# Optimization experiments

Hardware: AMD Instinct MI355X
Metric: run time of the kernel (lower is better)

Reference implementation:

```python
import jax, jax.numpy as jnp
import numpy as np

N_KEYS, PER_KEY = 8, 6
NUM_CONCEPTS = N_KEYS * PER_KEY  # 48
NUM_CLASS = 7
D_VIT, D = 768, 512
LOGIT_SCALE = 100.0


def adaptive_avg_pool_matrix(L_in: int, L_out: int) -> np.ndarray:
    """Linear operator replicating torch AdaptiveAvgPool1d: out[i] = mean(x[start_i:end_i])."""
    M = np.zeros((L_in, L_out), dtype=np.float32)
    for i in range(L_out):
        s = (i * L_in) // L_out
        e = -(((-(i + 1)) * L_in) // L_out)  # ceil((i+1)*L_in/L_out)
        M[s:e, i] = 1.0 / (e - s)
    return M


def setup_inputs() -> dict:
    key = jax.random.key(0)
    ks = jax.random.split(key, 12)
    feats = jax.random.normal(ks[0], (12, 32, 197, D_VIT), dtype=jnp.float32)
    # frozen text-side concept embeddings (CLIP text feats are ~unit norm, 512-d)
    ce = jax.random.normal(ks[1], (NUM_CONCEPTS, D), dtype=jnp.float32)
    concept_embeds = ce / jnp.linalg.norm(ce, axis=-1, keepdims=True)
    sc = 1.0 / np.sqrt(D_VIT)
    W_lin = jax.random.normal(ks[2], (D, D_VIT), dtype=jnp.float32) * sc
    b_lin = jnp.zeros((D,), dtype=jnp.float32)
    W_proj = jax.random.normal(ks[3], (D, D_VIT), dtype=jnp.float32) * sc
    scg = 1.0 / np.sqrt(3 * D)
    W_gate = jax.random.normal(ks[4], (D, 3 * D), dtype=jnp.float32) * scg
    b_gate = jnp.zeros((D,), dtype=jnp.float32)
    scu = 1.0 / np.sqrt(2 * D)
    W_upd = jax.random.normal(ks[5], (D, 2 * D), dtype=jnp.float32) * scu
    b_upd = jnp.zeros((D,), dtype=jnp.float32)
    W_cls = jax.random.normal(ks[6], (NUM_CLASS, NUM_CONCEPTS), dtype=jnp.float32) / np.sqrt(NUM_CONCEPTS)
    b_cls = jnp.zeros((NUM_CLASS,), dtype=jnp.float32)
    return {
        'feats': feats, 'concept_embeds': concept_embeds,
        'W_lin': W_lin, 'b_lin': b_lin, 'W_proj': W_proj,
        'W_gate': W_gate, 'b_gate': b_gate, 'W_upd': W_upd, 'b_upd': b_upd,
        'W_cls': W_cls, 'b_cls': b_cls,
    }


def _forward(feats, concept_embeds, W_lin, b_lin, W_proj, W_gate, b_gate, W_upd, b_upd, W_cls, b_cls):
    L, B, S, _ = feats.shape
    M = jnp.asarray(adaptive_avg_pool_matrix(S - 1, NUM_CONCEPTS))  # [196, 48]
    q0 = jnp.broadcast_to(concept_embeds[None], (B, NUM_CONCEPTS, D))

    def step(q, f):  # f: [B, 197, 768]
        cls_tok = f[:, :1, :]                                  # [B,1,768]
        pooled = jnp.einsum('bjd,ji->bid', f[:, 1:, :], M)     # [B,48,768]
        vt = jnp.concatenate([cls_tok, pooled], axis=1) @ W_lin.T + b_lin  # [B,49,512]
        attn = jax.nn.softmax(jnp.einsum('bqd,bvd->bqv', q, vt), axis=-1)
        fuse = jnp.einsum('bqv,bvd->bqd', attn, vt)            # [B,48,512]
        cls_ctx = jnp.broadcast_to(cls_tok @ W_proj.T, q.shape)
        gate = jax.nn.sigmoid(jnp.concatenate([fuse, q, cls_ctx], -1) @ W_gate.T + b_gate)
        upd = jnp.tanh(jnp.concatenate([fuse, q], -1) @ W_upd.T + b_upd)
        return gate * q + (1.0 - gate) * upd, fuse

    _, trace = jax.lax.scan(step, q0, feats)                   # trace: [12,B,48,512]

    last = trace[-1]
    vision_semantic = last / jnp.maximum(jnp.linalg.norm(last, axis=-1, keepdims=True), 1e-12)
    vs = vision_semantic.reshape(B, N_KEYS, PER_KEY, D)
    anchors = concept_embeds.reshape(N_KEYS, PER_KEY, D)
    image_logits = (LOGIT_SCALE * jnp.einsum('bkpd,kqd->bkpq', vs, anchors).mean(axis=2)).reshape(B, NUM_CONCEPTS)
    cls_logits = image_logits @ W_cls.T + b_cls
    diffs = trace[1:] - jax.lax.stop_gradient(trace[:-1])
    loss_consistency = jnp.sum(jnp.mean(diffs * diffs, axis=(1, 2, 3)))
    return cls_logits, image_logits, loss_consistency


def reference(feats, concept_embeds, W_lin, b_lin, W_proj, W_gate, b_gate, W_upd, b_upd, W_cls, b_cls):
    return _forward(feats, concept_embeds, W_lin, b_lin, W_proj, W_gate, b_gate, W_upd, b_upd, W_cls, b_cls)
```

## Files before the change

### kernel.cpp

```cpp
#include <hip/hip_runtime.h>
#include <hip/hip_bf16.h>

#define LL 12
#define BB 32
#define SS 197
#define DV 768
#define DD 512
#define CC 48
#define VV 49
#define LOSS_DEN 786432.0f

typedef unsigned short u16;
typedef unsigned int u32;
using bf16x8 = __attribute__((ext_vector_type(8))) __bf16;
using f32x4 = __attribute__((ext_vector_type(4))) float;
using u16x8 = __attribute__((ext_vector_type(8))) u16;

__device__ __forceinline__ u16 bf16h(float x) {
    u32 u = __builtin_bit_cast(u32, x);
    return (u16)((u + 0x7FFFu + ((u >> 16) & 1u)) >> 16);
}
__device__ __forceinline__ float bf2f(u16 h) {
    u32 u = ((u32)h) << 16;
    return __builtin_bit_cast(float, u);
}
__device__ __forceinline__ f32x4 mfma16(bf16x8 a, bf16x8 b, f32x4 c) {
    return __builtin_amdgcn_mfma_f32_16x16x32_bf16(a, b, c, 0, 0, 0);
}
__device__ __forceinline__ void gl_lds16(const void* g, void* s) {
    __builtin_amdgcn_global_load_lds((const __attribute__((address_space(1))) u32*)g,
                                     (__attribute__((address_space(3))) u32*)s, 16, 0, 0);
}

#define NLW (512 * 768)
#define NGW (512 * 1536)
#define NUW (512 * 1024)
#define POOL_BLKS (LL * BB * VV)
#define WSPLIT_BLKS ((NLW + NGW + NUW) / 256)
#define INITQ_BLKS ((BB * CC * DD) / 256)

__global__ __launch_bounds__(256) void mega_pre(const float* __restrict__ feats,
                                                const float* __restrict__ Wl,
                                                const float* __restrict__ Wg,
                                                const float* __restrict__ Wu,
                                                const float* __restrict__ ce,
                                                u16* __restrict__ Xh, u16* __restrict__ Xl,
                                                u16* Wlh, u16* Wll, u16* Wgh, u16* Wgl,
                                                u16* Wuh, u16* Wul,
                                                u16* __restrict__ qh, u16* __restrict__ ql,
                                                float* __restrict__ loss) {
    int bid = blockIdx.x;
    int t = threadIdx.x;
    if (bid < POOL_BLKS) {
        int row = bid;
        int v = row % VV;
        int lb = row / VV;
        const float* f = feats + (size_t)lb * SS * DV;
        for (int d = t; d < DV; d += 256) {
            float val;
            if (v == 0) {
                val = f[d];
            } else {
                int i = v - 1;
                int s = (i * 196) / 48;
                int e = ((i + 1) * 196 + 47) / 48;
                float acc = 0.0f;
                for (int j = s; j < e; ++j) acc += f[(size_t)(1 + j) * DV + d];
                val = acc / (float)(e - s);
            }
            u16 h = bf16h(val);
            Xh[(size_t)row * DV + d] = h;
            Xl[(size_t)row * DV + d] = bf16h(val - bf2f(h));
        }
    } else if (bid < POOL_BLKS + WSPLIT_BLKS) {
        int i = (bid - POOL_BLKS) * 256 + t;
        float v;
        u16 *ph, *pl;
        int j;
        if (i < NLW) { v = Wl[i]; ph = Wlh; pl = Wll; j = i; }
        else if (i < NLW + NGW) { j = i - NLW; v = Wg[j]; ph = Wgh; pl = Wgl; }
        else { j = i - NLW - NGW; v = Wu[j]; ph = Wuh; pl = Wul; }
        u16 hh = bf16h(v);
        ph[j] = hh;
        pl[j] = bf16h(v - bf2f(hh));
    } else {
        int i = (bid - POOL_BLKS - WSPLIT_BLKS) * 256 + t;
        float v = ce[i % (CC * DD)];
        u16 hh = bf16h(v);
        qh[i] = hh;
        ql[i] = bf16h(v - bf2f(hh));
        if (i == 0) loss[0] = 0.0f;
    }
}

__global__ __launch_bounds__(256) void gemm_f32(const float* __restrict__ A, int lda,
                                                const float* __restrict__ W, int wstride, int K,
                                                const float* __restrict__ bias,
                                                float* __restrict__ Cout) {
    __shared__ float As[32][65];
    __shared__ float Bs[32][65];
    int t = threadIdx.x;
    int m0 = blockIdx.x * 64;
    int n0 = blockIdx.y * 64;
    int r = t >> 2;
    int kc = (t & 3) * 8;
    int tx = t & 15, ty = t >> 4;
    float acc[4][4] = {};
    for (int k0 = 0; k0 < K; k0 += 32) {
        const float4* pa = (const float4*)(A + (size_t)(m0 + r) * lda + k0 + kc);
        float4 a0 = pa[0], a1 = pa[1];
        const float4* pw = (const float4*)(W + (size_t)(n0 + r) * wstride + k0 + kc);
        float4 w0 = pw[0], w1 = pw[1];
        As[kc + 0][r] = a0.x; As[kc + 1][r] = a0.y; As[kc + 2][r] = a0.z; As[kc + 3][r] = a0.w;
        As[kc + 4][r] = a1.x; As[kc + 5][r] = a1.y; As[kc + 6][r] = a1.z; As[kc + 7][r] = a1.w;
        Bs[kc + 0][r] = w0.x; Bs[kc + 1][r] = w0.y; Bs[kc + 2][r] = w0.z; Bs[kc + 3][r] = w0.w;
        Bs[kc + 4][r] = w1.x; Bs[kc + 5][r] = w1.y; Bs[kc + 6][r] = w1.z; Bs[kc + 7][r] = w1.w;
        __syncthreads();
#pragma unroll
        for (int kk = 0; kk < 32; ++kk) {
            float a[4], b[4];
#pragma unroll
            for (int i = 0; i < 4; ++i) { a[i] = As[kk][ty * 4 + i]; b[i] = Bs[kk][tx * 4 + i]; }
#pragma unroll
            for (int i = 0; i < 4; ++i)
#pragma unroll
                for (int j = 0; j < 4; ++j) acc[i][j] += a[i] * b[j];
        }
        __syncthreads();
    }
#pragma unroll
    for (int i = 0; i < 4; ++i) {
        int m = m0 + ty * 4 + i;
#pragma unroll
        for (int j = 0; j < 4; ++j) {
            int n = n0 + tx * 4 + j;
            Cout[(size_t)m * DD + n] = acc[i][j] + (bias ? bias[n] : 0.0f);
        }
    }
}

__global__ __launch_bounds__(256, 2) void vt_gemm(const u16* __restrict__ Xh, const u16* __restrict__ Xl,
                                                  const u16* __restrict__ Wh, const u16* __restrict__ Wl,
                                                  const float* __restrict__ bias,
                                                  u16* __restrict__ vthp, u16* __restrict__ vtlp) {
    __shared__ u16 sm[24576];
    int tid = threadIdx.x;
    int w = tid >> 6, l = tid & 63, lr = l & 15, ls = l >> 4;
    int i = blockIdx.x, m, n;
    if (i < 1152) { int a = i >> 6, r2 = i & 63; m = 8 * a + (r2 & 7); n = r2 >> 3; }
    else { int j = i - 1152; m = 144 + (j >> 3); n = j & 7; }
    int m0 = m * 128, n0 = n * 64;
    f32x4 acc[2][4];
#pragma unroll
    for (int ii = 0; ii < 2; ++ii)
#pragma unroll
        for (int j = 0; j < 4; ++j) acc[ii][j] = f32x4{0.f, 0.f, 0.f, 0.f};

    auto stage = [&](u16* dst, int k0) {
#pragma unroll
        for (int is = 0; is < 6; ++is) {
            int q = is * 256 + tid;
            const u16* src;
            int off;
            if (is < 2)      { int qr = q;        int row = qr >> 2, sl = qr & 3; src = Xh + (size_t)(m0 + row) * DV + k0 + ((sl ^ ((row >> 1) & 3)) << 3); off = qr * 8; }
            else if (is < 4) { int qr = q - 512;  int row = qr >> 2, sl = qr & 3; src = Xl + (size_t)(m0 + row) * DV + k0 + ((sl ^ ((row >> 1) & 3)) << 3); off = 4096 + qr * 8; }
            else if (is < 5) { int qr = q - 1024; int row = qr >> 2, sl = qr & 3; src = Wh + (size_t)(n0 + row) * DV + k0 + ((sl ^ ((row >> 1) & 3)) << 3); off = 8192 + qr * 8; }
            else             { int qr = q - 1280; int row = qr >> 2, sl = qr & 3; src = Wl + (size_t)(n0 + row) * DV + k0 + ((sl ^ ((row >> 1) & 3)) << 3); off = 10240 + qr * 8; }
            gl_lds16(src, dst + off);
        }
    };

    stage(sm, 0);
    __syncthreads();
    for (int t = 0; t < 24; ++t) {
        u16* cur = sm + ((t & 1) ? 12288 : 0);
        u16* nxt = sm + ((t & 1) ? 0 : 12288);
        if (t + 1 < 24) stage(nxt, (t + 1) * 32);
        bf16x8 ah[2], al2[2], bh[4], bl2[4];
#pragma unroll
        for (int rf = 0; rf < 2; ++rf) {
            int row = 32 * w + 16 * rf + lr;
            int ro = row * 32 + ((ls ^ ((row >> 1) & 3)) << 3);
            ah[rf] = *(const bf16x8*)(cur + ro);
            al2[rf] = *(const bf16x8*)(cur + 4096 + ro);
        }
#pragma unroll
        for (int cf = 0; cf < 4; ++cf) {
            int nn = 16 * cf + lr;
            int no = nn * 32 + ((ls ^ ((nn >> 1) & 3)) << 3);
            bh[cf] = *(const bf16x8*)(cur + 8192 + no);
            bl2[cf] = *(const bf16x8*)(cur + 10240 + no);
        }
#pragma unroll
        for (int rf = 0; rf < 2; ++rf)
#pragma unroll
            for (int cf = 0; cf < 4; ++cf) {
                acc[rf][cf] = mfma16(ah[rf], bh[cf], acc[rf][cf]);
                acc[rf][cf] = mfma16(ah[rf], bl2[cf], acc[rf][cf]);
                acc[rf][cf] = mfma16(al2[rf], bh[cf], acc[rf][cf]);
            }
        __syncthreads();
    }
#pragma unroll
    for (int rf = 0; rf < 2; ++rf)
#pragma unroll
        for (int cf = 0; cf < 4; ++cf)
#pragma unroll
            for (int r = 0; r < 4; ++r) {
                int row = m0 + 32 * w + 16 * rf + 4 * ls + r;
                int col = n0 + 16 * cf + lr;
                float v = acc[rf][cf][r] + bias[col];
                size_t o = (size_t)row * DD + col;
                u16 hh = bf16h(v);
                vthp[o] = hh;
                vtlp[o] = bf16h(v - bf2f(hh));
            }
}

__device__ __forceinline__ void gemm32x64(u16* sm, const u16* Ah, const u16* Al,
                                          const u16* Wgh, const u16* Wgl,
                                          const u16* Wuh, const u16* Wul,
                                          int m0, int n0, int colOff, int tid,
                                          f32x4 accg[2], f32x4 accu[2]) {
    int w = tid >> 6, lane = tid & 63, lr = lane & 15, ls = lane >> 4;
    auto stage = [&](u16* buf, int k0) {
        {
            int j = tid, row = j >> 3, sl = j & 7;
            int ko = k0 + ((sl ^ (row & 7)) << 3);
            gl_lds16(Ah + (size_t)(m0 + row) * DD + ko, buf + j * 8);
            gl_lds16(Al + (size_t)(m0 + row) * DD + ko, buf + 2048 + j * 8);
        }
#pragma unroll
        for (int i2 = 0; i2 < 8; ++i2) {
            int aidx = tid + 256 * i2;
            int arr = aidx >> 9, j = aidx & 511;
            int row = j >> 3, sl = j & 7;
            int ko = colOff + k0 + ((sl ^ (row & 7)) << 3);
            const u16* src;
            if (arr == 0) src = Wgh + (size_t)(n0 + row) * 1536 + ko;
            else if (arr == 1) src = Wgl + (size_t)(n0 + row) * 1536 + ko;
            else if (arr == 2) src = Wuh + (size_t)(n0 + row) * 1024 + ko;
            else src = Wul + (size_t)(n0 + row) * 1024 + ko;
            gl_lds16(src, buf + 4096 + arr * 4096 + j * 8);
        }
    };
    stage(sm, 0);
    __syncthreads();
    for (int t = 0; t < 8; ++t) {
        u16* cur = sm + (t & 1) * 20480;
        if (t + 1 < 8) stage(sm + ((t + 1) & 1) * 20480, (t + 1) * 64);
#pragma unroll
        for (int ks = 0; ks < 2; ++ks) {
            int slot = ks * 4 + ls;
            int n = 16 * w + lr;
            int bo = n * 64 + ((slot ^ (n & 7)) << 3);
            bf16x8 gh8 = *(const bf16x8*)(cur + 4096 + bo);
            bf16x8 gl8 = *(const bf16x8*)(cur + 8192 + bo);
            bf16x8 uh8 = *(const bf16x8*)(cur + 12288 + bo);
            bf16x8 ul8 = *(const bf16x8*)(cur + 16384 + bo);
#pragma unroll
            for (int rf = 0; rf < 2; ++rf) {
                int r = 16 * rf + lr;
                int ao = r * 64 + ((slot ^ (r & 7)) << 3);
                bf16x8 ah8 = *(const bf16x8*)(cur + ao);
                bf16x8 al8 = *(const bf16x8*)(cur + 2048 + ao);
                accg[rf] = mfma16(ah8, gh8, accg[rf]);
                accg[rf] = mfma16(ah8, gl8, accg[rf]);
                accg[rf] = mfma16(al8, gh8, accg[rf]);
                accu[rf] = mfma16(ah8, uh8, accu[rf]);
                accu[rf] = mfma16(ah8, ul8, accu[rf]);
                accu[rf] = mfma16(al8, uh8, accu[rf]);
            }
        }
        __syncthreads();
    }
}

__global__ __launch_bounds__(256, 2) void attn_qpart(
    const u16* __restrict__ qh, const u16* __restrict__ ql,
    const u16* __restrict__ vthL, const u16* __restrict__ vtlL,
    float* __restrict__ fcur, const float* __restrict__ fprev,
    u16* __restrict__ fh, u16* __restrict__ fl,
    float* __restrict__ loss, int do_loss,
    const u16* __restrict__ Wgh, const u16* __restrict__ Wgl,
    const u16* __restrict__ Wuh, const u16* __restrict__ Wul,
    float* __restrict__ qg, float* __restrict__ qu) {
    __shared__ u16 sm[40960];
    int tid = threadIdx.x;
    if (blockIdx.x < 192) {
        int wgid = blockIdx.x * 4 + (tid >> 6);
        int lane = tid & 63;
        int b = wgid / 24;
        int r0 = b * CC + (wgid % 24) * 2;
        size_t o0 = (size_t)r0 * DD + lane * 8;
        u16x8 h0 = *(const u16x8*)(qh + o0), g0 = *(const u16x8*)(ql + o0);
        u16x8 h1 = *(const u16x8*)(qh + o0 + DD), g1 = *(const u16x8*)(ql + o0 + DD);
        float q0v[8], q1v[8];
#pragma unroll
        for (int j = 0; j < 8; ++j) {
            q0v[j] = bf2f(h0[j]) + bf2f(g0[j]);
            q1v[j] = bf2f(h1[j]) + bf2f(g1[j]);
        }
        const u16* vh = vthL + (size_t)b * VV * DD + lane * 8;
        const u16* vl = vtlL + (size_t)b * VV * DD + lane * 8;
        float m0 = -3e38f, m1 = -3e38f, s0 = 0.f, s1 = 0.f;
        float a0[8] = {}, a1[8] = {};
        for (int v = 0; v < VV; ++v) {
            u16x8 rh = *(const u16x8*)(vh + v * DD);
            u16x8 rl = *(const u16x8*)(vl + v * DD);
            float rv[8];
#pragma unroll
            for (int j = 0; j < 8; ++j) rv[j] = bf2f(rh[j]) + bf2f(rl[j]);
            float p0 = 0.f, p1 = 0.f;
#pragma unroll
            for (int j = 0; j < 8; ++j) { p0 += q0v[j] * rv[j]; p1 += q1v[j] * rv[j]; }
#pragma unroll
            for (int off = 32; off > 0; off >>= 1) { p0 += __shfl_xor(p0, off); p1 += __shfl_xor(p1, off); }
            float nm0 = fmaxf(m0, p0);
            float sc0 = __expf(m0 - nm0), w0 = __expf(p0 - nm0);
            s0 = s0 * sc0 + w0;
            float nm1 = fmaxf(m1, p1);
            float sc1 = __expf(m1 - nm1), w1 = __expf(p1 - nm1);
            s1 = s1 * sc1 + w1;
#pragma unroll
            for (int j = 0; j < 8; ++j) {
                a0[j] = a0[j] * sc0 + w0 * rv[j];
                a1[j] = a1[j] * sc1 + w1 * rv[j];
            }
            m0 = nm0;
            m1 = nm1;
        }
        float inv0 = 1.0f / s0, inv1 = 1.0f / s1;
        float d2 = 0.f;
        float f0v[8], f1v[8];
        u16x8 oh0, ol0, oh1, ol1;
#pragma unroll
        for (int j = 0; j < 8; ++j) {
            float f = a0[j] * inv0;
            f0v[j] = f;
            u16 hh = bf16h(f);
            oh0[j] = hh;
            ol0[j] = bf16h(f - bf2f(hh));
            float f2 = a1[j] * inv1;
            f1v[j] = f2;
            u16 h2 = bf16h(f2);
            oh1[j] = h2;
            ol1[j] = bf16h(f2 - bf2f(h2));
        }
        *(float4*)(fcur + o0) = float4{f0v[0], f0v[1], f0v[2], f0v[3]};
        *(float4*)(fcur + o0 + 4) = float4{f0v[4], f0v[5], f0v[6], f0v[7]};
        *(float4*)(fcur + o0 + DD) = float4{f1v[0], f1v[1], f1v[2], f1v[3]};
        *(float4*)(fcur + o0 + DD + 4) = float4{f1v[4], f1v[5], f1v[6], f1v[7]};
        *(u16x8*)(fh + o0) = oh0;
        *(u16x8*)(fl + o0) = ol0;
        *(u16x8*)(fh + o0 + DD) = oh1;
        *(u16x8*)(fl + o0 + DD) = ol1;
        if (do_loss) {
#pragma unroll
            for (int j = 0; j < 8; ++j) {
                float d = f0v[j] - fprev[o0 + j];
                d2 += d * d;
                float e = f1v[j] - fprev[o0 + DD + j];
                d2 += e * e;
            }
#pragma unroll
            for (int off = 32; off > 0; off >>= 1) d2 += __shfl_xor(d2, off);
            if (lane == 0) atomicAdd(loss, d2);
        }
    } else {
        int tb = blockIdx.x - 192;
        int m0 = (tb >> 3) * 32, n0 = (tb & 7) * 64;
        f32x4 accg[2], accu[2];
#pragma unroll
        for (int i = 0; i < 2; ++i) { accg[i] = f32x4{0.f, 0.f, 0.f, 0.f}; accu[i] = f32x4{0.f, 0.f, 0.f, 0.f}; }
        gemm32x64(sm, qh, ql, Wgh, Wgl, Wuh, Wul, m0, n0, 512, tid, accg, accu);
        int w = tid >> 6, lane = tid & 63, lr = lane & 15, ls = lane >> 4;
#pragma unroll
        for (int rf = 0; rf < 2; ++rf)
#pragma unroll
            for (int r = 0; r < 4; ++r) {
                int row = m0 + 16 * rf + 4 * ls + r;
                int col = n0 + 16 * w + lr;
                size_t o = (size_t)row * DD + col;
                qg[o] = accg[rf][r];
                qu[o] = accu[rf][r];
            }
    }
}

__global__ __launch_bounds__(256, 2) void fusepart(
    const u16* __restrict__ fhp, const u16* __restrict__ flp,
    const u16* __restrict__ qhp, const u16* __restrict__ qlp,
    const u16* __restrict__ Wgh, const u16* __restrict__ Wgl,
    const u16* __restrict__ Wuh, const u16* __restrict__ Wul,
    const float* __restrict__ qg, const float* __restrict__ qu,
    const float* __restrict__ CgL, const float* __restrict__ bu,
    u16* __restrict__ qoh, u16* __restrict__ qol) {
    __shared__ u16 sm[40960];
    int tid = threadIdx.x;
    int m0 = (blockIdx.x >> 3) * 32, n0 = (blockIdx.x & 7) * 64;
    f32x4 accg[2], accu[2];
#pragma unroll
    for (int i = 0; i < 2; ++i) { accg[i] = f32x4{0.f, 0.f, 0.f, 0.f}; accu[i] = f32x4{0.f, 0.f, 0.f, 0.f}; }
    gemm32x64(sm, fhp, flp, Wgh, Wgl, Wuh, Wul, m0, n0, 0, tid, accg, accu);
    int w = tid >> 6, lane = tid & 63, lr = lane & 15, ls = lane >> 4;
#pragma unroll
    for (int rf = 0; rf < 2; ++rf)
#pragma unroll
        for (int r = 0; r < 4; ++r) {
            int row = m0 + 16 * rf + 4 * ls + r;
            int col = n0 + 16 * w + lr;
            int b = row / CC;
            size_t o = (size_t)row * DD + col;
            float gpre = accg[rf][r] + qg[o] + CgL[(size_t)b * DD + col];
            float upre = accu[rf][r] + qu[o] + bu[col];
            float g = 1.0f / (1.0f + __expf(-gpre));
            float u = tanhf(upre);
            float qv = bf2f(qhp[o]) + bf2f(qlp[o]);
            float qo = g * qv + (1.0f - g) * u;
            u16 hh = bf16h(qo);
            qoh[o] = hh;
            qol[o] = bf16h(qo - bf2f(hh));
        }
}

__global__ __launch_bounds__(256) void final_kernel(const float* __restrict__ fuse_last,
                                                    const float* __restrict__ ce,
                                                    const float* __restrict__ W_cls,
                                                    const float* __restrict__ b_cls,
                                                    const float* __restrict__ loss_acc,
                                                    float* __restrict__ out) {
    int b = blockIdx.x;
    int t = threadIdx.x;
    int w = t >> 6, lane = t & 63;
    __shared__ float invn[CC];
    __shared__ float img[CC];
    const float* fb = fuse_last + (size_t)b * CC * DD;
    for (int c = w; c < CC; c += 4) {
        const float* fr = fb + (size_t)c * DD + lane * 8;
        float4 a0 = *(const float4*)fr;
        float4 a1 = *(const float4*)(fr + 4);
        float ss = a0.x * a0.x + a0.y * a0.y + a0.z * a0.z + a0.w * a0.w +
                   a1.x * a1.x + a1.y * a1.y + a1.z * a1.z + a1.w * a1.w;
#pragma unroll
        for (int off = 32; off > 0; off >>= 1) ss += __shfl_xor(ss, off);
        if (lane == 0) invn[c] = 1.0f / fmaxf(sqrtf(ss), 1e-12f);
    }
    __syncthreads();
    for (int g = w; g < CC; g += 4) {
        int k = g / 6;
        const float* ar = ce + (size_t)g * DD + lane * 8;
        float4 c0 = *(const float4*)ar;
        float4 c1 = *(const float4*)(ar + 4);
        float av[8] = {c0.x, c0.y, c0.z, c0.w, c1.x, c1.y, c1.z, c1.w};
        float accp = 0.0f;
        for (int p = 0; p < 6; ++p) {
            int row = k * 6 + p;
            const float* fr = fb + (size_t)row * DD + lane * 8;
            float4 f0 = *(const float4*)fr;
            float4 f1 = *(const float4*)(fr + 4);
            float fv[8] = {f0.x, f0.y, f0.z, f0.w, f1.x, f1.y, f1.z, f1.w};
            float d = 0.0f;
#pragma unroll
            for (int j = 0; j < 8; ++j) d += fv[j] * av[j];
            accp += d * invn[row];
        }
#pragma unroll
        for (int off = 32; off > 0; off >>= 1) accp += __shfl_xor(accp, off);
        if (lane == 0) img[g] = accp * (100.0f / 6.0f);
    }
    __syncthreads();
    if (t < CC) out[BB * 7 + b * CC + t] = img[t];
    if (t < 7) {
        float sacc = b_cls[t];
        for (int c = 0; c < CC; ++c) sacc += img[c] * W_cls[t * CC + c];
        out[b * 7 + t] = sacc;
    }
    if (b == 0 && t == 0) out[BB * 7 + BB * CC] = loss_acc[0] * (1.0f / LOSS_DEN);
}

extern "C" void kernel_launch(void* const* d_in, const int* in_sizes, int n_in,
                              void* d_out, int out_size, void* d_ws, size_t ws_size,
                              hipStream_t stream) {
    const float* feats = (const float*)d_in[0];
    const float* ce = (const float*)d_in[1];
    const float* W_lin = (const float*)d_in[2];
    const float* b_lin = (const float*)d_in[3];
    const float* W_proj = (const float*)d_in[4];
    const float* W_gate = (const float*)d_in[5];
    const float* b_gate = (const float*)d_in[6];
    const float* W_upd = (const float*)d_in[7];
    const float* b_upd = (const float*)d_in[8];
    const float* W_cls = (const float*)d_in[9];
    const float* b_cls = (const float*)d_in[10];
    float* out = (float*)d_out;

    char* base = (char*)d_ws;
    size_t off = 0;
    auto alloc = [&](size_t bytes) -> char* {
        char* r = base + off;
        off += (bytes + 255) & ~(size_t)255;
        return r;
    };
    u16* Xh = (u16*)alloc((size_t)LL * BB * VV * DV * 2);
    u16* Xl = (u16*)alloc((size_t)LL * BB * VV * DV * 2);
    u16* vth = (u16*)alloc((size_t)LL * BB * VV * DD * 2);
    u16* vtl = (u16*)alloc((size_t)LL * BB * VV * DD * 2);
    float* ctx = (float*)alloc((size_t)LL * BB * DD * 4);
    float* Cg = (float*)alloc((size_t)LL * BB * DD * 4);
    float* fbuf0 = (float*)alloc((size_t)BB * CC * DD * 4);
    float* fbuf1 = (float*)alloc((size_t)BB * CC * DD * 4);
    float* qg = (float*)alloc((size_t)BB * CC * DD * 4);
    float* qu = (float*)alloc((size_t)BB * CC * DD * 4);
    float* loss = (float*)alloc(256);
    u16* Wlh = (u16*)alloc((size_t)NLW * 2);
    u16* Wll = (u16*)alloc((size_t)NLW * 2);
    u16* Wgh = (u16*)alloc((size_t)NGW * 2);
    u16* Wgl = (u16*)alloc((size_t)NGW * 2);
    u16* Wuh = (u16*)alloc((size_t)NUW * 2);
    u16* Wul = (u16*)alloc((size_t)NUW * 2);
    u16* fh = (u16*)alloc((size_t)BB * CC * DD * 2);
    u16* fl = (u16*)alloc((size_t)BB * CC * DD * 2);
    u16* qah = (u16*)alloc((size_t)BB * CC * DD * 2);
    u16* qal = (u16*)alloc((size_t)BB * CC * DD * 2);
    u16* qbh = (u16*)alloc((size_t)BB * CC * DD * 2);
    u16* qbl = (u16*)alloc((size_t)BB * CC * DD * 2);
    u16* qph[2] = {qah, qbh};
    u16* qpl[2] = {qal, qbl};

    mega_pre<<<POOL_BLKS + WSPLIT_BLKS + INITQ_BLKS, 256, 0, stream>>>(
        feats, W_lin, W_gate, W_upd, ce, Xh, Xl, Wlh, Wll, Wgh, Wgl, Wuh, Wul, qah, qal, loss);
    {
        dim3 g(LL * BB / 64, DD / 64);
        gemm_f32<<<g, 256, 0, stream>>>(feats, SS * DV, W_proj, DV, DV, nullptr, ctx);
        gemm_f32<<<g, 256, 0, stream>>>(ctx, DD, W_gate + 1024, 1536, DD, b_gate, Cg);
    }
    vt_gemm<<<1176, 256, 0, stream>>>(Xh, Xl, Wlh, Wll, b_lin, vth, vtl);

    int qc = 0;
    for (int l = 0; l < LL; ++l) {
        float* fcur = (l & 1) ? fbuf1 : fbuf0;
        const float* fprev = (l & 1) ? fbuf0 : fbuf1;
        int grid = (l < LL - 1) ? 576 : 192;
        attn_qpart<<<grid, 256, 0, stream>>>(qph[qc], qpl[qc],
                                             vth + (size_t)l * BB * VV * DD, vtl + (size_t)l * BB * VV * DD,
                                             fcur, fprev, fh, fl, loss, l > 0 ? 1 : 0,
                                             Wgh, Wgl, Wuh, Wul, qg, qu);
        if (l < LL - 1) {
            fusepart<<<384, 256, 0, stream>>>(fh, fl, qph[qc], qpl[qc],
                                              Wgh, Wgl, Wuh, Wul, qg, qu,
                                              Cg + (size_t)l * BB * DD, b_upd,
                                              qph[qc ^ 1], qpl[qc ^ 1]);
            qc ^= 1;
        }
    }

    final_kernel<<<BB, 256, 0, stream>>>((LL - 1) & 1 ? fbuf1 : fbuf0, ce, W_cls, b_cls, loss, out);
}
```

Before: 940.2 us.

## Fold ctx/Cg GEMMs into pre and vt kernels; one query row per wavefront

New measurement: 2.781 ms. 2.96x slower.

```diff
diff --git a/kernel.cpp b/kernel.cpp
--- a/kernel.cpp
+++ b/kernel.cpp
@@ -38,17 +38,65 @@
 #define POOL_BLKS (LL * BB * VV)
 #define WSPLIT_BLKS ((NLW + NGW + NUW) / 256)
 #define INITQ_BLKS ((BB * CC * DD) / 256)
+#define CTX_BLKS 48
+
+__device__ __forceinline__ void gemm_f32_tile(const float* __restrict__ A, int lda,
+                                              const float* __restrict__ W, int wstride, int K,
+                                              const float* __restrict__ bias,
+                                              float* __restrict__ Cout,
+                                              int m0, int n0, int t, float* AsB, float* BsB) {
+    float (*As)[65] = (float(*)[65])AsB;
+    float (*Bs)[65] = (float(*)[65])BsB;
+    int r = t >> 2;
+    int kc = (t & 3) * 8;
+    int tx = t & 15, ty = t >> 4;
+    float acc[4][4] = {};
+    for (int k0 = 0; k0 < K; k0 += 32) {
+        const float4* pa = (const float4*)(A + (size_t)(m0 + r) * lda + k0 + kc);
+        float4 a0 = pa[0], a1 = pa[1];
+        const float4* pw = (const float4*)(W + (size_t)(n0 + r) * wstride + k0 + kc);
+        float4 w0 = pw[0], w1 = pw[1];
+        As[kc + 0][r] = a0.x; As[kc + 1][r] = a0.y; As[kc + 2][r] = a0.z; As[kc + 3][r] = a0.w;
+        As[kc + 4][r] = a1.x; As[kc + 5][r] = a1.y; As[kc + 6][r] = a1.z; As[kc + 7][r] = a1.w;
+        Bs[kc + 0][r] = w0.x; Bs[kc + 1][r] = w0.y; Bs[kc + 2][r] = w0.z; Bs[kc + 3][r] = w0.w;
+        Bs[kc + 4][r] = w1.x; Bs[kc + 5][r] = w1.y; Bs[kc + 6][r] = w1.z; Bs[kc + 7][r] = w1.w;
+        __syncthreads();
+#pragma unroll
+        for (int kk = 0; kk < 32; ++kk) {
+            float a[4], b[4];
+#pragma unroll
+            for (int i = 0; i < 4; ++i) { a[i] = As[kk][ty * 4 + i]; b[i] = Bs[kk][tx * 4 + i]; }
+#pragma unroll
+            for (int i = 0; i < 4; ++i)
+#pragma unroll
+                for (int j = 0; j < 4; ++j) acc[i][j] += a[i] * b[j];
+        }
+        __syncthreads();
+    }
+#pragma unroll
+    for (int i = 0; i < 4; ++i) {
+        int m = m0 + ty * 4 + i;
+#pragma unroll
+        for (int j = 0; j < 4; ++j) {
+            int n = n0 + tx * 4 + j;
+            Cout[(size_t)m * DD + n] = acc[i][j] + (bias ? bias[n] : 0.0f);
+        }
+    }
+}
 
 __global__ __launch_bounds__(256) void mega_pre(const float* __restrict__ feats,
                                                 const float* __restrict__ Wl,
                                                 const float* __restrict__ Wg,
                                                 const float* __restrict__ Wu,
+                                                const float* __restrict__ Wp,
                                                 const float* __restrict__ ce,
                                                 u16* __restrict__ Xh, u16* __restrict__ Xl,
                                                 u16* Wlh, u16* Wll, u16* Wgh, u16* Wgl,
                                                 u16* Wuh, u16* Wul,
                                                 u16* __restrict__ qh, u16* __restrict__ ql,
-                                                float* __restrict__ loss) {
+                                                float* __restrict__ loss,
+                                                float* __restrict__ ctx) {
+    __shared__ float smf[2 * 32 * 65];
     int bid = blockIdx.x;
     int t = threadIdx.x;
     if (bid < POOL_BLKS) {
@@ -83,68 +131,36 @@
         u16 hh = bf16h(v);
         ph[j] = hh;
         pl[j] = bf16h(v - bf2f(hh));
-    } else {
+    } else if (bid < POOL_BLKS + WSPLIT_BLKS + INITQ_BLKS) {
         int i = (bid - POOL_BLKS - WSPLIT_BLKS) * 256 + t;
         float v = ce[i % (CC * DD)];
         u16 hh = bf16h(v);
         qh[i] = hh;
         ql[i] = bf16h(v - bf2f(hh));
         if (i == 0) loss[0] = 0.0f;
-    }
-}
-
-__global__ __launch_bounds__(256) void gemm_f32(const float* __restrict__ A, int lda,
-                                                const float* __restrict__ W, int wstride, int K,
-                                                const float* __restrict__ bias,
-                                                float* __restrict__ Cout) {
-    __shared__ float As[32][65];
-    __shared__ float Bs[32][65];
-    int t = threadIdx.x;
-    int m0 = blockIdx.x * 64;
-    int n0 = blockIdx.y * 64;
-    int r = t >> 2;
-    int kc = (t & 3) * 8;
-    int tx = t & 15, ty = t >> 4;
-    float acc[4][4] = {};
-    for (int k0 = 0; k0 < K; k0 += 32) {
-        const float4* pa = (const float4*)(A + (size_t)(m0 + r) * lda + k0 + kc);
-        float4 a0 = pa[0], a1 = pa[1];
-        const float4* pw = (const float4*)(W + (size_t)(n0 + r) * wstride + k0 + kc);
-        float4 w0 = pw[0], w1 = pw[1];
-        As[kc + 0][r] = a0.x; As[kc + 1][r] = a0.y; As[kc + 2][r] = a0.z; As[kc + 3][r] = a0.w;
-        As[kc + 4][r] = a1.x; As[kc + 5][r] = a1.y; As[kc + 6][r] = a1.z; As[kc + 7][r] = a1.w;
-        Bs[kc + 0][r] = w0.x; Bs[kc + 1][r] = w0.y; Bs[kc + 2][r] = w0.z; Bs[kc + 3][r] = w0.w;
-        Bs[kc + 4][r] = w1.x; Bs[kc + 5][r] = w1.y; Bs[kc + 6][r] = w1.z; Bs[kc + 7][r] = w1.w;
-        __syncthreads();
-#pragma unroll
-        for (int kk = 0; kk < 32; ++kk) {
-            float a[4], b[4];
-#pragma unroll
-            for (int i = 0; i < 4; ++i) { a[i] = As[kk][ty * 4 + i]; b[i] = Bs[kk][tx * 4 + i]; }
-#pragma unroll
-            for (int i = 0; i < 4; ++i)
-#pragma unroll
-                for (int j = 0; j < 4; ++j) acc[i][j] += a[i] * b[j];
-        }
-        __syncthreads();
-    }
-#pragma unroll
-    for (int i = 0; i < 4; ++i) {
-        int m = m0 + ty * 4 + i;
-#pragma unroll
-        for (int j = 0; j < 4; ++j) {
-            int n = n0 + tx * 4 + j;
-            Cout[(size_t)m * DD + n] = acc[i][j] + (bias ? bias[n] : 0.0f);
-        }
-    }
-}
-
-__global__ __launch_bounds__(256, 2) void vt_gemm(const u16* __restrict__ Xh, const u16* __restrict__ Xl,
-                                                  const u16* __restrict__ Wh, const u16* __restrict__ Wl,
-                                                  const float* __restrict__ bias,
-                                                  u16* __restrict__ vthp, u16* __restrict__ vtlp) {
+    } else {
+        int b2 = bid - POOL_BLKS - WSPLIT_BLKS - INITQ_BLKS;
+        gemm_f32_tile(feats, SS * DV, Wp, DV, DV, nullptr, ctx,
+                      (b2 >> 3) * 64, (b2 & 7) * 64, t, smf, smf + 32 * 65);
+    }
+}
+
+__global__ __launch_bounds__(256, 2) void vtcg_gemm(const u16* __restrict__ Xh, const u16* __restrict__ Xl,
+                                                    const u16* __restrict__ Wh, const u16* __restrict__ Wl,
+                                                    const float* __restrict__ bias,
+                                                    u16* __restrict__ vthp, u16* __restrict__ vtlp,
+                                                    const float* __restrict__ ctx,
+                                                    const float* __restrict__ Wg,
+                                                    const float* __restrict__ bg,
+                                                    float* __restrict__ Cg) {
     __shared__ u16 sm[24576];
     int tid = threadIdx.x;
+    if (blockIdx.x >= 1176) {
+        int b2 = blockIdx.x - 1176;
+        gemm_f32_tile(ctx, DD, Wg + 1024, 1536, DD, bg, Cg,
+                      (b2 >> 3) * 64, (b2 & 7) * 64, tid, (float*)sm, (float*)sm + 32 * 65);
+        return;
+    }
     int w = tid >> 6, l = tid & 63, lr = l & 15, ls = l >> 4;
     int i = blockIdx.x, m, n;
     if (i < 1152) { int a = i >> 6, r2 = i & 63; m = 8 * a + (r2 & 7); n = r2 >> 3; }
@@ -287,88 +303,71 @@
     float* __restrict__ qg, float* __restrict__ qu) {
     __shared__ u16 sm[40960];
     int tid = threadIdx.x;
-    if (blockIdx.x < 192) {
-        int wgid = blockIdx.x * 4 + (tid >> 6);
+    if (blockIdx.x < 384) {
+        int row = blockIdx.x * 4 + (tid >> 6);
         int lane = tid & 63;
-        int b = wgid / 24;
-        int r0 = b * CC + (wgid % 24) * 2;
-        size_t o0 = (size_t)r0 * DD + lane * 8;
+        int b = row / CC;
+        size_t o0 = (size_t)row * DD + lane * 8;
         u16x8 h0 = *(const u16x8*)(qh + o0), g0 = *(const u16x8*)(ql + o0);
-        u16x8 h1 = *(const u16x8*)(qh + o0 + DD), g1 = *(const u16x8*)(ql + o0 + DD);
-        float q0v[8], q1v[8];
-#pragma unroll
-        for (int j = 0; j < 8; ++j) {
-            q0v[j] = bf2f(h0[j]) + bf2f(g0[j]);
-            q1v[j] = bf2f(h1[j]) + bf2f(g1[j]);
-        }
+        float qv[8];
+#pragma unroll
+        for (int j = 0; j < 8; ++j) qv[j] = bf2f(h0[j]) + bf2f(g0[j]);
         const u16* vh = vthL + (size_t)b * VV * DD + lane * 8;
         const u16* vl = vtlL + (size_t)b * VV * DD + lane * 8;
-        float m0 = -3e38f, m1 = -3e38f, s0 = 0.f, s1 = 0.f;
-        float a0[8] = {}, a1[8] = {};
+        float p[VV];
+#pragma unroll
         for (int v = 0; v < VV; ++v) {
             u16x8 rh = *(const u16x8*)(vh + v * DD);
             u16x8 rl = *(const u16x8*)(vl + v * DD);
-            float rv[8];
-#pragma unroll
-            for (int j = 0; j < 8; ++j) rv[j] = bf2f(rh[j]) + bf2f(rl[j]);
-            float p0 = 0.f, p1 = 0.f;
-#pragma unroll
-            for (int j = 0; j < 8; ++j) { p0 += q0v[j] * rv[j]; p1 += q1v[j] * rv[j]; }
-#pragma unroll
-            for (int off = 32; off > 0; off >>= 1) { p0 += __shfl_xor(p0, off); p1 += __shfl_xor(p1, off); }
-            float nm0 = fmaxf(m0, p0);
-            float sc0 = __expf(m0 - nm0), w0 = __expf(p0 - nm0);
-            s0 = s0 * sc0 + w0;
-            float nm1 = fmaxf(m1, p1);
-            float sc1 = __expf(m1 - nm1), w1 = __expf(p1 - nm1);
-            s1 = s1 * sc1 + w1;
+            float d = 0.f;
+#pragma unroll
+            for (int j = 0; j < 8; ++j) d += qv[j] * (bf2f(rh[j]) + bf2f(rl[j]));
+#pragma unroll
+            for (int off = 32; off > 0; off >>= 1) d += __shfl_xor(d, off);
+            p[v] = d;
+        }
+        float mx = -3e38f;
+#pragma unroll
+        for (int v = 0; v < VV; ++v) mx = fmaxf(mx, p[v]);
+        float s = 0.f;
+#pragma unroll
+        for (int v = 0; v < VV; ++v) { p[v] = __expf(p[v] - mx); s += p[v]; }
+        float inv = 1.0f / s;
+        float acc[8] = {};
+#pragma unroll
+        for (int v = 0; v < VV; ++v) {
+            u16x8 rh = *(const u16x8*)(vh + v * DD);
+            u16x8 rl = *(const u16x8*)(vl + v * DD);
+#pragma unroll
+            for (int j = 0; j < 8; ++j) acc[j] += p[v] * (bf2f(rh[j]) + bf2f(rl[j]));
+        }
+        float fv[8];
+        u16x8 oh, ol;
+#pragma unroll
+        for (int j = 0; j < 8; ++j) {
+            float f = acc[j] * inv;
+            fv[j] = f;
+            u16 hh = bf16h(f);
+            oh[j] = hh;
+            ol[j] = bf16h(f - bf2f(hh));
+        }
+        *(float4*)(fcur + o0) = float4{fv[0], fv[1], fv[2], fv[3]};
+        *(float4*)(fcur + o0 + 4) = float4{fv[4], fv[5], fv[6], fv[7]};
+        *(u16x8*)(fh + o0) = oh;
+        *(u16x8*)(fl + o0) = ol;
+        if (do_loss) {
+            float d2 = 0.f;
 #pragma unroll
             for (int j = 0; j < 8; ++j) {
-                a0[j] = a0[j] * sc0 + w0 * rv[j];
-                a1[j] = a1[j] * sc1 + w1 * rv[j];
-            }
-            m0 = nm0;
-            m1 = nm1;
-        }
-        float inv0 = 1.0f / s0, inv1 = 1.0f / s1;
-        float d2 = 0.f;
-        float f0v[8], f1v[8];
-        u16x8 oh0, ol0, oh1, ol1;
-#pragma unroll
-        for (int j = 0; j < 8; ++j) {
-            float f = a0[j] * inv0;
-            f0v[j] = f;
-            u16 hh = bf16h(f);
-            oh0[j] = hh;
-            ol0[j] = bf16h(f - bf2f(hh));
-            float f2 = a1[j] * inv1;
-            f1v[j] = f2;
-            u16 h2 = bf16h(f2);
-            oh1[j] = h2;
-            ol1[j] = bf16h(f2 - bf2f(h2));
-        }
-        *(float4*)(fcur + o0) = float4{f0v[0], f0v[1], f0v[2], f0v[3]};
-        *(float4*)(fcur + o0 + 4) = float4{f0v[4], f0v[5], f0v[6], f0v[7]};
-        *(float4*)(fcur + o0 + DD) = float4{f1v[0], f1v[1], f1v[2], f1v[3]};
-        *(float4*)(fcur + o0 + DD + 4) = float4{f1v[4], f1v[5], f1v[6], f1v[7]};
-        *(u16x8*)(fh + o0) = oh0;
-        *(u16x8*)(fl + o0) = ol0;
-        *(u16x8*)(fh + o0 + DD) = oh1;
-        *(u16x8*)(fl + o0 + DD) = ol1;
-        if (do_loss) {
-#pragma unroll
-            for (int j = 0; j < 8; ++j) {
-                float d = f0v[j] - fprev[o0 + j];
+                float d = fv[j] - fprev[o0 + j];
                 d2 += d * d;
-                float e = f1v[j] - fprev[o0 + DD + j];
-                d2 += e * e;
             }
 #pragma unroll
             for (int off = 32; off > 0; off >>= 1) d2 += __shfl_xor(d2, off);
             if (lane == 0) atomicAdd(loss, d2);
         }
     } else {
-        int tb = blockIdx.x - 192;
+        int tb = blockIdx.x - 384;
         int m0 = (tb >> 3) * 32, n0 = (tb & 7) * 64;
         f32x4 accg[2], accu[2];
 #pragma unroll
@@ -416,8 +415,8 @@
             float upre = accu[rf][r] + qu[o] + bu[col];
             float g = 1.0f / (1.0f + __expf(-gpre));
             float u = tanhf(upre);
-            float qv = bf2f(qhp[o]) + bf2f(qlp[o]);
-            float qo = g * qv + (1.0f - g) * u;
+            float qvv = bf2f(qhp[o]) + bf2f(qlp[o]);
+            float qo = g * qvv + (1.0f - g) * u;
             u16 hh = bf16h(qo);
             qoh[o] = hh;
             qol[o] = bf16h(qo - bf2f(hh));
@@ -528,20 +527,17 @@
     u16* qph[2] = {qah, qbh};
     u16* qpl[2] = {qal, qbl};
 
-    mega_pre<<<POOL_BLKS + WSPLIT_BLKS + INITQ_BLKS, 256, 0, stream>>>(
-        feats, W_lin, W_gate, W_upd, ce, Xh, Xl, Wlh, Wll, Wgh, Wgl, Wuh, Wul, qah, qal, loss);
-    {
-        dim3 g(LL * BB / 64, DD / 64);
-        gemm_f32<<<g, 256, 0, stream>>>(feats, SS * DV, W_proj, DV, DV, nullptr, ctx);
-        gemm_f32<<<g, 256, 0, stream>>>(ctx, DD, W_gate + 1024, 1536, DD, b_gate, Cg);
-    }
-    vt_gemm<<<1176, 256, 0, stream>>>(Xh, Xl, Wlh, Wll, b_lin, vth, vtl);
+    mega_pre<<<POOL_BLKS + WSPLIT_BLKS + INITQ_BLKS + CTX_BLKS, 256, 0, stream>>>(
+        feats, W_lin, W_gate, W_upd, W_proj, ce, Xh, Xl, Wlh, Wll, Wgh, Wgl, Wuh, Wul,
+        qah, qal, loss, ctx);
+    vtcg_gemm<<<1176 + CTX_BLKS, 256, 0, stream>>>(Xh, Xl, Wlh, Wll, b_lin, vth, vtl,
+                                                   ctx, W_gate, b_gate, Cg);
 
     int qc = 0;
     for (int l = 0; l < LL; ++l) {
         float* fcur = (l & 1) ? fbuf1 : fbuf0;
         const float* fprev = (l & 1) ? fbuf0 : fbuf1;
-        int grid = (l < LL - 1) ? 576 : 192;
+        int grid = (l < LL - 1) ? 768 : 384;
         attn_qpart<<<grid, 256, 0, stream>>>(qph[qc], qpl[qc],
                                              vth + (size_t)l * BB * VV * DD, vtl + (size_t)l * BB * VV * DD,
                                              fcur, fprev, fh, fl, loss, l > 0 ? 1 : 0,
```
